# Kernel optimization log

Measured on AMD Instinct MI355X. Metric: run time of the kernel, lower is better.

The kernel has to match this reference:

```python
import jax, jax.numpy as jnp
import numpy as np

EPSILON = 1e-4
MAX_ITER = 10


def setup_inputs() -> dict:
    key = jax.random.key(0)
    k1, k2, k3 = jax.random.split(key, 3)
    B, N, M = 64, 1024, 1024
    s = jax.random.uniform(k1, (B, N, M), dtype=jnp.float32)
    nrows = jax.random.randint(k2, (B,), 0, N, dtype=jnp.int32)
    ncols = jax.random.randint(k3, (B,), 0, M, dtype=jnp.int32)
    return {"s": s, "nrows": nrows, "ncols": ncols}


def reference(s, nrows, ncols):
    # s: [B, N, M]; nrows/ncols: [B] valid row/col counts per sample.
    B, N, M = s.shape
    row_mask = jnp.arange(N, dtype=nrows.dtype)[None, :] < nrows[:, None]  # [B, N]
    col_mask = jnp.arange(M, dtype=ncols.dtype)[None, :] < ncols[:, None]  # [B, M]
    mask = row_mask[:, :, None] & col_mask[:, None, :]  # [B, N, M]

    s = s + EPSILON
    for i in range(MAX_ITER):
        # i even -> column normalization (sum over dim 1); i odd -> row normalization (sum over dim 2)
        axis = 2 if i % 2 == 1 else 1
        ssum = jnp.sum(s, axis=axis, keepdims=True)
        tmp = jnp.where(mask, 1.0 / ssum, jnp.zeros((), dtype=s.dtype))
        s = s * tmp
    return s
```

## Files before the change

### kernel.cpp

```cpp
#include <hip/hip_runtime.h>

#define EPS 1e-4f

constexpr int Bn = 64;
constexpr int Nn = 1024;
constexpr int Mn = 1024;
constexpr int NSPLIT = 16;
constexpr int CHUNK  = Nn / NSPLIT;
constexpr int SLOT0  = 2 * NSPLIT;
constexpr int SLOT1  = 64;

__device__ __forceinline__ unsigned pk2(float a, float b) {
    unsigned ua = __float_as_uint(a); ua = (ua + 0x7fffu + ((ua >> 16) & 1u)) >> 16;
    unsigned ub = __float_as_uint(b); ub = (ub + 0x7fffu + ((ub >> 16) & 1u)) >> 16;
    return ua | (ub << 16);
}
__device__ __forceinline__ float lo16(unsigned v) { return __uint_as_float(v << 16); }
__device__ __forceinline__ float hi16(unsigned v) { return __uint_as_float(v & 0xffff0000u); }

__global__ __launch_bounds__(256) void fuse0_kernel(
        const float* __restrict__ s, unsigned short* __restrict__ sc,
        float* __restrict__ p) {
    const int b = blockIdx.x, sp = blockIdx.y;
    const int t = threadIdx.x, half = t >> 7, tc = t & 127;
    float acc[8];
    #pragma unroll
    for (int k = 0; k < 8; ++k) acc[k] = 0.f;
    for (int j = 0; j < CHUNK; j += 2) {
        const int n = sp * CHUNK + j + half;
        const size_t roff = ((size_t)b * Nn + n) * Mn;
        const float4* src = reinterpret_cast<const float4*>(s + roff) + 2 * tc;
        float4 v0 = src[0], v1 = src[1];
        v0.x += EPS; v0.y += EPS; v0.z += EPS; v0.w += EPS;
        v1.x += EPS; v1.y += EPS; v1.z += EPS; v1.w += EPS;
        acc[0] += v0.x; acc[1] += v0.y; acc[2] += v0.z; acc[3] += v0.w;
        acc[4] += v1.x; acc[5] += v1.y; acc[6] += v1.z; acc[7] += v1.w;
        uint4 w = { pk2(v0.x, v0.y), pk2(v0.z, v0.w),
                    pk2(v1.x, v1.y), pk2(v1.z, v1.w) };
        reinterpret_cast<uint4*>(sc + roff)[tc] = w;
    }
    float* pp = p + ((size_t)(b * SLOT1 + sp * 2 + half)) * Mn + tc * 8;
    float4 o0 = {acc[0], acc[1], acc[2], acc[3]};
    float4 o1 = {acc[4], acc[5], acc[6], acc[7]};
    *reinterpret_cast<float4*>(pp)     = o0;
    *reinterpret_cast<float4*>(pp + 4) = o1;
}

__global__ __launch_bounds__(256) void col_final_kernel(
        const float* __restrict__ p, const int* __restrict__ ncols,
        float* __restrict__ c, int slots) {
    const int b = blockIdx.x;
    const int m0 = threadIdx.x << 2;
    float sx = 0.f, sy = 0.f, sz = 0.f, sw = 0.f;
    for (int k = 0; k < slots; ++k) {
        float4 v = *reinterpret_cast<const float4*>(
            p + ((size_t)(b * SLOT1 + k)) * Mn + m0);
        sx += v.x; sy += v.y; sz += v.z; sw += v.w;
    }
    const int nc = ncols[b];
    float4 o;
    o.x = (m0 + 0 < nc && sx > 0.f) ? 1.f / sx : 0.f;
    o.y = (m0 + 1 < nc && sy > 0.f) ? 1.f / sy : 0.f;
    o.z = (m0 + 2 < nc && sz > 0.f) ? 1.f / sz : 0.f;
    o.w = (m0 + 3 < nc && sw > 0.f) ? 1.f / sw : 0.f;
    *reinterpret_cast<float4*>(c + (size_t)b * Mn + m0) = o;
}

__global__ __launch_bounds__(256) void rowcol_kernel(
        const unsigned short* __restrict__ sc, const float* __restrict__ c,
        const int* __restrict__ nrows, float* __restrict__ p) {
    const int b = blockIdx.x;
    const int t = threadIdx.x, w = t >> 6, l = t & 63;
    const int n0 = blockIdx.y * 64 + w * 16;
    const float4* cb = reinterpret_cast<const float4*>(c + (size_t)b * Mn);
    const float4 c0 = cb[2 * l], c1 = cb[2 * l + 1];
    const float4 c2 = cb[128 + 2 * l], c3 = cb[128 + 2 * l + 1];
    const int nr = nrows[b];
    float acc[16];
    #pragma unroll
    for (int k = 0; k < 16; ++k) acc[k] = 0.f;
    for (int j = 0; j < 16; ++j) {
        const int n = n0 + j;
        const uint4* row = reinterpret_cast<const uint4*>(sc + ((size_t)b * Nn + n) * Mn);
        uint4 a = row[l], d = row[64 + l];
        const float v0 = lo16(a.x), v1 = hi16(a.x), v2 = lo16(a.y), v3 = hi16(a.y);
        const float v4 = lo16(a.z), v5 = hi16(a.z), v6 = lo16(a.w), v7 = hi16(a.w);
        const float v8 = lo16(d.x), v9 = hi16(d.x), v10 = lo16(d.y), v11 = hi16(d.y);
        const float v12 = lo16(d.z), v13 = hi16(d.z), v14 = lo16(d.w), v15 = hi16(d.w);
        float part = v0 * c0.x + v1 * c0.y + v2 * c0.z + v3 * c0.w
                   + v4 * c1.x + v5 * c1.y + v6 * c1.z + v7 * c1.w
                   + v8 * c2.x + v9 * c2.y + v10 * c2.z + v11 * c2.w
                   + v12 * c3.x + v13 * c3.y + v14 * c3.z + v15 * c3.w;
        #pragma unroll
        for (int off = 1; off < 64; off <<= 1) part += __shfl_xor(part, off, 64);
        const float rv = (n < nr && part > 0.f) ? 1.f / part : 0.f;
        acc[0]  += v0 * rv;  acc[1]  += v1 * rv;  acc[2]  += v2 * rv;  acc[3]  += v3 * rv;
        acc[4]  += v4 * rv;  acc[5]  += v5 * rv;  acc[6]  += v6 * rv;  acc[7]  += v7 * rv;
        acc[8]  += v8 * rv;  acc[9]  += v9 * rv;  acc[10] += v10 * rv; acc[11] += v11 * rv;
        acc[12] += v12 * rv; acc[13] += v13 * rv; acc[14] += v14 * rv; acc[15] += v15 * rv;
    }
    float* pp = p + ((size_t)(b * SLOT1) + blockIdx.y * 4 + w) * Mn;
    float4 o;
    o = {acc[0], acc[1], acc[2], acc[3]};     *reinterpret_cast<float4*>(pp + 8 * l)           = o;
    o = {acc[4], acc[5], acc[6], acc[7]};     *reinterpret_cast<float4*>(pp + 8 * l + 4)       = o;
    o = {acc[8], acc[9], acc[10], acc[11]};   *reinterpret_cast<float4*>(pp + 512 + 8 * l)     = o;
    o = {acc[12], acc[13], acc[14], acc[15]}; *reinterpret_cast<float4*>(pp + 512 + 8 * l + 4) = o;
}

__global__ __launch_bounds__(256) void final_kernel(
        const float* __restrict__ s, const float* __restrict__ c,
        const int* __restrict__ nrows, float* __restrict__ out) {
    const int b = blockIdx.x;
    const int t = threadIdx.x, w = t >> 6, l = t & 63;
    const int n0 = blockIdx.y * 32 + w * 8;
    const float4* cb = reinterpret_cast<const float4*>(c + (size_t)b * Mn);
    float4 cc[4];
    #pragma unroll
    for (int k = 0; k < 4; ++k) cc[k] = cb[64 * k + l];
    const int nr = nrows[b];
    for (int j = 0; j < 8; ++j) {
        const int n = n0 + j;
        const size_t roff = ((size_t)b * Nn + n) * Mn;
        const float4* row = reinterpret_cast<const float4*>(s + roff);
        float4 a[4];
        float part = 0.f;
        #pragma unroll
        for (int k = 0; k < 4; ++k) {
            a[k] = row[64 * k + l];
            a[k].x += EPS; a[k].y += EPS; a[k].z += EPS; a[k].w += EPS;
            part += a[k].x * cc[k].x + a[k].y * cc[k].y
                  + a[k].z * cc[k].z + a[k].w * cc[k].w;
        }
        #pragma unroll
        for (int off = 1; off < 64; off <<= 1) part += __shfl_xor(part, off, 64);
        const float rv = (n < nr && part > 0.f) ? 1.f / part : 0.f;
        float4* orow = reinterpret_cast<float4*>(out + roff);
        #pragma unroll
        for (int k = 0; k < 4; ++k) {
            float4 o;
            o.x = a[k].x * cc[k].x * rv;
            o.y = a[k].y * cc[k].y * rv;
            o.z = a[k].z * cc[k].z * rv;
            o.w = a[k].w * cc[k].w * rv;
            orow[64 * k + l] = o;
        }
    }
}

extern "C" void kernel_launch(void* const* d_in, const int* in_sizes, int n_in,
                              void* d_out, int out_size, void* d_ws, size_t ws_size,
                              hipStream_t stream) {
    const float* s     = (const float*)d_in[0];
    const int*   nrows = (const int*)d_in[1];
    const int*   ncols = (const int*)d_in[2];
    float* out = (float*)d_out;

    unsigned short* sc = (unsigned short*)d_ws;
    float* p = (float*)(sc + (size_t)Bn * Nn * Mn);
    float* c = p + (size_t)Bn * SLOT1 * Mn;

    fuse0_kernel<<<dim3(Bn, NSPLIT), 256, 0, stream>>>(s, sc, p);
    col_final_kernel<<<Bn, 256, 0, stream>>>(p, ncols, c, SLOT0);
    for (int it = 0; it < 4; ++it) {
        rowcol_kernel<<<dim3(Bn, Nn / 64), 256, 0, stream>>>(sc, c, nrows, p);
        col_final_kernel<<<Bn, 256, 0, stream>>>(p, ncols, c, SLOT1);
    }
    final_kernel<<<dim3(Bn, Nn / 32), 256, 0, stream>>>(s, c, nrows, out);
}
```

Before: 716.4 us.

## Skip masked rows and columns in bf16 Sinkhorn passes and widen col reduction

Uses nrows/ncols to skip loading and storing data outside the valid region. fuse0 stores the bf16 copy only for valid rows, rowcol breaks early past nrows and skips column segments past ncols, and final_kernel writes zeros for invalid rows without reading the input. col_final now spreads each batch across 4 blocks with scalar loads to get more parallelism. With random sizes about half the rows and columns are masked, so memory traffic should drop a lot. The added per-row branching stays warp-uniform.

```diff
diff --git a/kernel.cpp b/kernel.cpp
--- a/kernel.cpp
+++ b/kernel.cpp
@@ -20,9 +20,10 @@
 
 __global__ __launch_bounds__(256) void fuse0_kernel(
         const float* __restrict__ s, unsigned short* __restrict__ sc,
-        float* __restrict__ p) {
+        float* __restrict__ p, const int* __restrict__ nrows) {
     const int b = blockIdx.x, sp = blockIdx.y;
     const int t = threadIdx.x, half = t >> 7, tc = t & 127;
+    const int nr = nrows[b];
     float acc[8];
     #pragma unroll
     for (int k = 0; k < 8; ++k) acc[k] = 0.f;
@@ -35,9 +36,11 @@
         v1.x += EPS; v1.y += EPS; v1.z += EPS; v1.w += EPS;
         acc[0] += v0.x; acc[1] += v0.y; acc[2] += v0.z; acc[3] += v0.w;
         acc[4] += v1.x; acc[5] += v1.y; acc[6] += v1.z; acc[7] += v1.w;
-        uint4 w = { pk2(v0.x, v0.y), pk2(v0.z, v0.w),
-                    pk2(v1.x, v1.y), pk2(v1.z, v1.w) };
-        reinterpret_cast<uint4*>(sc + roff)[tc] = w;
+        if (n < nr) {
+            uint4 w = { pk2(v0.x, v0.y), pk2(v0.z, v0.w),
+                        pk2(v1.x, v1.y), pk2(v1.z, v1.w) };
+            reinterpret_cast<uint4*>(sc + roff)[tc] = w;
+        }
     }
     float* pp = p + ((size_t)(b * SLOT1 + sp * 2 + half)) * Mn + tc * 8;
     float4 o0 = {acc[0], acc[1], acc[2], acc[3]};
@@ -50,39 +53,37 @@
         const float* __restrict__ p, const int* __restrict__ ncols,
         float* __restrict__ c, int slots) {
     const int b = blockIdx.x;
-    const int m0 = threadIdx.x << 2;
-    float sx = 0.f, sy = 0.f, sz = 0.f, sw = 0.f;
-    for (int k = 0; k < slots; ++k) {
-        float4 v = *reinterpret_cast<const float4*>(
-            p + ((size_t)(b * SLOT1 + k)) * Mn + m0);
-        sx += v.x; sy += v.y; sz += v.z; sw += v.w;
-    }
+    const int m = blockIdx.y * 256 + threadIdx.x;
+    float sum = 0.f;
+    for (int k = 0; k < slots; ++k)
+        sum += p[((size_t)(b * SLOT1 + k)) * Mn + m];
     const int nc = ncols[b];
-    float4 o;
-    o.x = (m0 + 0 < nc && sx > 0.f) ? 1.f / sx : 0.f;
-    o.y = (m0 + 1 < nc && sy > 0.f) ? 1.f / sy : 0.f;
-    o.z = (m0 + 2 < nc && sz > 0.f) ? 1.f / sz : 0.f;
-    o.w = (m0 + 3 < nc && sw > 0.f) ? 1.f / sw : 0.f;
-    *reinterpret_cast<float4*>(c + (size_t)b * Mn + m0) = o;
+    c[(size_t)b * Mn + m] = (m < nc && sum > 0.f) ? 1.f / sum : 0.f;
 }
 
 __global__ __launch_bounds__(256) void rowcol_kernel(
         const unsigned short* __restrict__ sc, const float* __restrict__ c,
-        const int* __restrict__ nrows, float* __restrict__ p) {
+        const int* __restrict__ nrows, const int* __restrict__ ncols,
+        float* __restrict__ p) {
     const int b = blockIdx.x;
     const int t = threadIdx.x, w = t >> 6, l = t & 63;
     const int n0 = blockIdx.y * 64 + w * 16;
+    const int nr = nrows[b], nc = ncols[b];
     const float4* cb = reinterpret_cast<const float4*>(c + (size_t)b * Mn);
     const float4 c0 = cb[2 * l], c1 = cb[2 * l + 1];
     const float4 c2 = cb[128 + 2 * l], c3 = cb[128 + 2 * l + 1];
-    const int nr = nrows[b];
+    const bool lo_ok = (8 * l) < nc;
+    const bool hi_ok = (512 + 8 * l) < nc;
+    const uint4 z4 = {0u, 0u, 0u, 0u};
     float acc[16];
     #pragma unroll
     for (int k = 0; k < 16; ++k) acc[k] = 0.f;
     for (int j = 0; j < 16; ++j) {
         const int n = n0 + j;
+        if (n >= nr) break;
         const uint4* row = reinterpret_cast<const uint4*>(sc + ((size_t)b * Nn + n) * Mn);
-        uint4 a = row[l], d = row[64 + l];
+        uint4 a = lo_ok ? row[l] : z4;
+        uint4 d = hi_ok ? row[64 + l] : z4;
         const float v0 = lo16(a.x), v1 = hi16(a.x), v2 = lo16(a.y), v3 = hi16(a.y);
         const float v4 = lo16(a.z), v5 = hi16(a.z), v6 = lo16(a.w), v7 = hi16(a.w);
         const float v8 = lo16(d.x), v9 = hi16(d.x), v10 = lo16(d.y), v11 = hi16(d.y);
@@ -93,7 +94,7 @@
                    + v12 * c3.x + v13 * c3.y + v14 * c3.z + v15 * c3.w;
         #pragma unroll
         for (int off = 1; off < 64; off <<= 1) part += __shfl_xor(part, off, 64);
-        const float rv = (n < nr && part > 0.f) ? 1.f / part : 0.f;
+        const float rv = (part > 0.f) ? 1.f / part : 0.f;
         acc[0]  += v0 * rv;  acc[1]  += v1 * rv;  acc[2]  += v2 * rv;  acc[3]  += v3 * rv;
         acc[4]  += v4 * rv;  acc[5]  += v5 * rv;  acc[6]  += v6 * rv;  acc[7]  += v7 * rv;
         acc[8]  += v8 * rv;  acc[9]  += v9 * rv;  acc[10] += v10 * rv; acc[11] += v11 * rv;
@@ -109,32 +110,43 @@
 
 __global__ __launch_bounds__(256) void final_kernel(
         const float* __restrict__ s, const float* __restrict__ c,
-        const int* __restrict__ nrows, float* __restrict__ out) {
+        const int* __restrict__ nrows, const int* __restrict__ ncols,
+        float* __restrict__ out) {
     const int b = blockIdx.x;
     const int t = threadIdx.x, w = t >> 6, l = t & 63;
     const int n0 = blockIdx.y * 32 + w * 8;
+    const int nr = nrows[b], nc = ncols[b];
     const float4* cb = reinterpret_cast<const float4*>(c + (size_t)b * Mn);
     float4 cc[4];
+    bool ok[4];
     #pragma unroll
-    for (int k = 0; k < 4; ++k) cc[k] = cb[64 * k + l];
-    const int nr = nrows[b];
+    for (int k = 0; k < 4; ++k) {
+        cc[k] = cb[64 * k + l];
+        ok[k] = (256 * k + 4 * l) < nc;
+    }
+    const float4 zf = {0.f, 0.f, 0.f, 0.f};
     for (int j = 0; j < 8; ++j) {
         const int n = n0 + j;
         const size_t roff = ((size_t)b * Nn + n) * Mn;
+        float4* orow = reinterpret_cast<float4*>(out + roff);
+        if (n >= nr) {
+            #pragma unroll
+            for (int k = 0; k < 4; ++k) orow[64 * k + l] = zf;
+            continue;
+        }
         const float4* row = reinterpret_cast<const float4*>(s + roff);
         float4 a[4];
         float part = 0.f;
         #pragma unroll
         for (int k = 0; k < 4; ++k) {
-            a[k] = row[64 * k + l];
+            a[k] = ok[k] ? row[64 * k + l] : zf;
             a[k].x += EPS; a[k].y += EPS; a[k].z += EPS; a[k].w += EPS;
             part += a[k].x * cc[k].x + a[k].y * cc[k].y
                   + a[k].z * cc[k].z + a[k].w * cc[k].w;
         }
         #pragma unroll
         for (int off = 1; off < 64; off <<= 1) part += __shfl_xor(part, off, 64);
-        const float rv = (n < nr && part > 0.f) ? 1.f / part : 0.f;
-        float4* orow = reinterpret_cast<float4*>(out + roff);
+        const float rv = (part > 0.f) ? 1.f / part : 0.f;
         #pragma unroll
         for (int k = 0; k < 4; ++k) {
             float4 o;
@@ -159,11 +171,11 @@
     float* p = (float*)(sc + (size_t)Bn * Nn * Mn);
     float* c = p + (size_t)Bn * SLOT1 * Mn;
 
-    fuse0_kernel<<<dim3(Bn, NSPLIT), 256, 0, stream>>>(s, sc, p);
-    col_final_kernel<<<Bn, 256, 0, stream>>>(p, ncols, c, SLOT0);
+    fuse0_kernel<<<dim3(Bn, NSPLIT), 256, 0, stream>>>(s, sc, p, nrows);
+    col_final_kernel<<<dim3(Bn, 4), 256, 0, stream>>>(p, ncols, c, SLOT0);
     for (int it = 0; it < 4; ++it) {
-        rowcol_kernel<<<dim3(Bn, Nn / 64), 256, 0, stream>>>(sc, c, nrows, p);
-        col_final_kernel<<<Bn, 256, 0, stream>>>(p, ncols, c, SLOT1);
+        rowcol_kernel<<<dim3(Bn, Nn / 64), 256, 0, stream>>>(sc, c, nrows, ncols, p);
+        col_final_kernel<<<dim3(Bn, 4), 256, 0, stream>>>(p, ncols, c, SLOT1);
     }
-    final_kernel<<<dim3(Bn, Nn / 32), 256, 0, stream>>>(s, c, nrows, out);
+    final_kernel<<<dim3(Bn, Nn / 32), 256, 0, stream>>>(s, c, nrows, ncols, out);
 }
```

Result: no change. 727.0 us (+1.5%).
